# Kernel optimization log

Hardware: AMD Instinct MI355X
Metric: run time of the kernel (lower is better)

Reference implementation:

```python
import jax, jax.numpy as jnp
import numpy as np

N_USERS = 100000
N_ITEMS = 100000
EMB = 64
N_NODES = N_USERS + N_ITEMS + 2  # +1 padding row each for users and items
N_EDGES = 1200000
N_BEHAVIORS = 3
LAYERS = [3, 3, 3]
EPS = 1e-12  # F.normalize eps


def setup_inputs() -> dict:
    key = jax.random.key(0)
    k1, k2, k3, k4, k5 = jax.random.split(key, 5)
    user_emb = jax.random.normal(k1, (N_USERS + 1, EMB), dtype=jnp.float32)
    item_emb = jax.random.normal(k2, (N_ITEMS + 1, EMB), dtype=jnp.float32)
    rows = jax.random.randint(k3, (N_BEHAVIORS, N_EDGES), 0, N_NODES, dtype=jnp.int32)
    cols = jax.random.randint(k4, (N_BEHAVIORS, N_EDGES), 0, N_NODES, dtype=jnp.int32)
    weights = jax.random.uniform(k5, (N_BEHAVIORS, N_EDGES), dtype=jnp.float32)
    return {"user_emb": user_emb, "item_emb": item_emb, "rows": rows,
            "cols": cols, "weights": weights}


def _spmm(rows_b, cols_b, w_b, x):
    # sparse [N,N] @ dense [N,D] via gather + segment-sum (COO SpMM)
    msg = x[cols_b] * w_b[:, None]                      # [E, D]
    return jax.ops.segment_sum(msg, rows_b, num_segments=N_NODES)


def _l2_normalize(x):
    norm = jnp.sqrt(jnp.sum(x * x, axis=-1, keepdims=True))
    return x / jnp.maximum(norm, EPS)


def reference(user_emb, item_emb, rows, cols, weights):
    # NSED.gcn_propagate: sequential LightGCN per behavior with residual chaining
    total = jnp.concatenate([user_emb, item_emb], axis=0)  # [N, D]
    outs = []
    for b in range(N_BEHAVIORS):
        x = total
        acc = x            # running sum of layer embeddings (== mean of stack)
        for _ in range(LAYERS[b]):
            x = _spmm(rows[b], cols[b], weights[b], x)
            acc = acc + x
        lightgcn_emb = acc / jnp.float32(LAYERS[b] + 1)    # stack+mean over layers
        total = _l2_normalize(lightgcn_emb) + total
        outs.append(total)
    return jnp.stack(outs, axis=0)  # [B, N, D]
```

## Files before the change

### kernel.cpp

```cpp
#include <hip/hip_runtime.h>
#include <math.h>

#define N_USERS 100000
#define N_ITEMS 100000
#define EMB 64
#define N_NODES (N_USERS + N_ITEMS + 2)
#define N_EDGES 1200000
#define E3 (3 * N_EDGES)
#define N3 (3 * N_NODES)
#define ND ((long)N_NODES * (long)EMB)

#define KPB 1024
#define NBUCKET ((N3 + KPB - 1) / KPB)
#define CAP 6656
#define EPB 8192
#define SCT 512
#define NB_P1 ((E3 + EPB - 1) / EPB)

typedef float f32x4 __attribute__((ext_vector_type(4)));
typedef float f32x8 __attribute__((ext_vector_type(8)));
typedef unsigned short u16x4 __attribute__((ext_vector_type(4)));
typedef unsigned short u16x8 __attribute__((ext_vector_type(8)));

__device__ inline unsigned short f2bf(float f) {
    unsigned int u = __float_as_uint(f);
    return (unsigned short)((u + 0x7FFFu + ((u >> 16) & 1u)) >> 16);
}
__device__ inline void fma8(f32x8& acc, float w, u16x8 s) {
    #pragma unroll
    for (int j = 0; j < 8; ++j)
        acc[j] = fmaf(w, __uint_as_float((unsigned int)s[j] << 16), acc[j]);
}
__device__ inline f32x8 bf8_to_f8(u16x8 s) {
    f32x8 f;
    #pragma unroll
    for (int j = 0; j < 8; ++j) f[j] = __uint_as_float((unsigned int)s[j] << 16);
    return f;
}
__device__ inline u16x8 f8_to_bf8(f32x8 f) {
    u16x8 s;
    #pragma unroll
    for (int j = 0; j < 8; ++j) s[j] = f2bf(f[j]);
    return s;
}

__global__ void make_tb_kernel(const float4* __restrict__ u,
                               const float4* __restrict__ it,
                               u16x4* __restrict__ tb) {
    long i = (long)blockIdx.x * blockDim.x + threadIdx.x;
    if (i >= ND / 4) return;
    long n = i >> 4;
    float4 v = (n < (long)(N_USERS + 1)) ? u[i] : it[i - (long)(N_USERS + 1) * 16];
    u16x4 b;
    b.x = f2bf(v.x); b.y = f2bf(v.y); b.z = f2bf(v.z); b.w = f2bf(v.w);
    tb[i] = b;
}

__global__ void init_bcur_kernel(int* __restrict__ bcur, unsigned int* __restrict__ sedge) {
    int i = blockIdx.x * blockDim.x + threadIdx.x;
    if (i < NBUCKET) bcur[i] = i * CAP;
    if (i < 16) sedge[E3 + i] = 0u;
}

__global__ void bucket_scatter_kernel(const int* __restrict__ rows,
                                      const int* __restrict__ cols,
                                      const float* __restrict__ w,
                                      int* __restrict__ bcur,
                                      int2* __restrict__ tmpedge) {
    __shared__ int h[NBUCKET];
    __shared__ int lbase[NBUCKET];
    for (int i = threadIdx.x; i < NBUCKET; i += SCT) h[i] = 0;
    __syncthreads();
    long base = (long)blockIdx.x * EPB;
    int keys[EPB / SCT];
    for (int k = 0; k < EPB / SCT; ++k) {
        long e = base + k * SCT + threadIdx.x;
        int key = -1;
        if (e < E3) {
            int b = (e >= 2L * N_EDGES) ? 2 : ((e >= N_EDGES) ? 1 : 0);
            key = b * N_NODES + rows[e];
            atomicAdd(&h[key / KPB], 1);
        }
        keys[k] = key;
    }
    __syncthreads();
    for (int i = threadIdx.x; i < NBUCKET; i += SCT) {
        int c = h[i];
        lbase[i] = c ? atomicAdd(&bcur[i], c) : 0;
        h[i] = 0;
    }
    __syncthreads();
    for (int k = 0; k < EPB / SCT; ++k) {
        long e = base + k * SCT + threadIdx.x;
        int key = keys[k];
        if (key >= 0) {
            int bk = key / KPB;
            int pos = lbase[bk] + atomicAdd(&h[bk], 1);
            int2 pk;
            pk.x = ((key & (KPB - 1)) << 18) | cols[e];
            pk.y = __float_as_int(w[e]);
            tmpedge[pos] = pk;
        }
    }
}

__global__ void bucket_scan_kernel(const int* __restrict__ bcur, int* __restrict__ bbase,
                                   int* __restrict__ rowptr) {
    __shared__ int sm[1024];
    __shared__ int carry;
    int tid = threadIdx.x;
    if (tid == 0) carry = 0;
    __syncthreads();
    for (int base = 0; base < NBUCKET; base += 1024) {
        int i = base + tid;
        int v = (i < NBUCKET) ? (bcur[i] - i * CAP) : 0;
        sm[tid] = v;
        __syncthreads();
        for (int off = 1; off < 1024; off <<= 1) {
            int t = (tid >= off) ? sm[tid - off] : 0;
            __syncthreads();
            sm[tid] += t;
            __syncthreads();
        }
        if (i < NBUCKET) bbase[i] = sm[tid] - v + carry;
        __syncthreads();
        if (tid == 0) carry += sm[1023];
        __syncthreads();
    }
    if (tid == 0) { bbase[NBUCKET] = E3; rowptr[N3] = E3; }
}

__global__ void bucket_sort_kernel(const int* __restrict__ bbase,
                                   const int2* __restrict__ tmpedge,
                                   unsigned int* __restrict__ sedge,
                                   int* __restrict__ rowptr) {
    int g = blockIdx.x;
    int s = bbase[g];
    int cnt = bbase[g + 1] - s;
    long tb = (long)g * CAP;
    __shared__ int h[KPB];
    __shared__ int ex[KPB];
    __shared__ int tmp[512];
    int tid = threadIdx.x;
    h[tid * 2] = 0; h[tid * 2 + 1] = 0;
    __syncthreads();
    for (int i = tid; i < cnt; i += 512) atomicAdd(&h[tmpedge[tb + i].x >> 18], 1);
    __syncthreads();
    int a0 = h[tid * 2], a1 = h[tid * 2 + 1];
    int psum = a0 + a1;
    tmp[tid] = psum;
    __syncthreads();
    for (int off = 1; off < 512; off <<= 1) {
        int t = (tid >= off) ? tmp[tid - off] : 0;
        __syncthreads();
        tmp[tid] += t;
        __syncthreads();
    }
    int pex = tmp[tid] - psum;
    ex[tid * 2] = pex;
    ex[tid * 2 + 1] = pex + a0;
    __syncthreads();
    for (int j = tid; j < KPB; j += 512) {
        int key = g * KPB + j;
        if (key < N3) rowptr[key] = s + ex[j];
    }
    h[tid * 2] = ex[tid * 2];
    h[tid * 2 + 1] = ex[tid * 2 + 1];
    __syncthreads();
    for (int i = tid; i < cnt; i += 512) {
        int2 pk = tmpedge[tb + i];
        int kl = pk.x >> 18;
        int pos = s + atomicAdd(&h[kl], 1);
        float w = __int_as_float(pk.y);
        int wq = (int)fmaf(w, 16384.f, 0.5f);
        wq = wq > 16383 ? 16383 : (wq < 0 ? 0 : wq);
        sedge[pos] = ((unsigned int)(pk.x & 0x3FFFF) << 14) | (unsigned int)wq;
    }
}

__global__ void spmm_bf16_kernel(const int* __restrict__ rowptr,
                                 const unsigned int* __restrict__ sedge,
                                 const u16x8* __restrict__ x,
                                 u16x8* __restrict__ y) {
    int wid  = threadIdx.x >> 6;
    int lane = threadIdx.x & 63;
    int r = lane >> 3;
    int q = lane & 7;
    int n = (blockIdx.x * 4 + wid) * 8 + r;
    if (n >= N_NODES) return;
    int s = rowptr[n], e = rowptr[n + 1];
    f32x8 acc = {0.f, 0.f, 0.f, 0.f, 0.f, 0.f, 0.f, 0.f};
    for (int base = s; ; base += 8) {
        unsigned int ee[8];
        u16x8 bb[8];
        float ww[8];
        #pragma unroll
        for (int j = 0; j < 8; ++j) ee[j] = sedge[base + j];
        #pragma unroll
        for (int j = 0; j < 8; ++j) {
            bool valid = (base + j) < e;
            int c = valid ? (int)(ee[j] >> 14) : 0;
            ww[j] = valid ? (float)(ee[j] & 16383u) * (1.0f / 16384.0f) : 0.f;
            bb[j] = x[(long)c * 8 + q];
        }
        #pragma unroll
        for (int j = 0; j < 8; ++j) fma8(acc, ww[j], bb[j]);
        if (base + 8 >= e) break;
    }
    __builtin_nontemporal_store(f8_to_bf8(acc), &y[(long)n * 8 + q]);
}

__global__ void spmm_final_kernel(const int* __restrict__ rowptr,
                                  const unsigned int* __restrict__ sedge,
                                  const u16x8* __restrict__ Qb,
                                  const float* __restrict__ Tin,
                                  const float* __restrict__ uemb,
                                  const float* __restrict__ iemb,
                                  const u16x8* __restrict__ Pb,
                                  float* __restrict__ outp,
                                  u16x8* __restrict__ TbOut) {
    int wid  = threadIdx.x >> 6;
    int lane = threadIdx.x & 63;
    int r = lane >> 3;
    int q = lane & 7;
    int n = (blockIdx.x * 4 + wid) * 8 + r;
    if (n >= N_NODES) return;
    int s = rowptr[n], e = rowptr[n + 1];
    f32x8 acc = {0.f, 0.f, 0.f, 0.f, 0.f, 0.f, 0.f, 0.f};
    for (int base = s; ; base += 8) {
        unsigned int ee[8];
        u16x8 bb[8];
        float ww[8];
        #pragma unroll
        for (int j = 0; j < 8; ++j) ee[j] = sedge[base + j];
        #pragma unroll
        for (int j = 0; j < 8; ++j) {
            bool valid = (base + j) < e;
            int c = valid ? (int)(ee[j] >> 14) : 0;
            ww[j] = valid ? (float)(ee[j] & 16383u) * (1.0f / 16384.0f) : 0.f;
            bb[j] = Qb[(long)c * 8 + q];
        }
        #pragma unroll
        for (int j = 0; j < 8; ++j) fma8(acc, ww[j], bb[j]);
        if (base + 8 >= e) break;
    }
    const float* tsrc;
    if (Tin) tsrc = Tin + (long)n * EMB;
    else if (n <= N_USERS) tsrc = uemb + (long)n * EMB;
    else tsrc = iemb + (long)(n - N_USERS - 1) * EMB;
    long o = (long)n * 8 + q;
    f32x8 t = *(const f32x8*)(tsrc + q * 8);
    f32x8 p = bf8_to_f8(Pb[o]);
    f32x8 qv = bf8_to_f8(Qb[o]);
    f32x8 v;
    float ss = 0.f;
    #pragma unroll
    for (int j = 0; j < 8; ++j) {
        v[j] = (t[j] + p[j] + qv[j] + acc[j]) * 0.25f;
        ss = fmaf(v[j], v[j], ss);
    }
    ss += __shfl_xor(ss, 1, 64);
    ss += __shfl_xor(ss, 2, 64);
    ss += __shfl_xor(ss, 4, 64);
    float inv = 1.0f / fmaxf(sqrtf(ss), 1e-12f);
    f32x8 ov;
    #pragma unroll
    for (int j = 0; j < 8; ++j) ov[j] = fmaf(v[j], inv, t[j]);
    __builtin_nontemporal_store(ov, (f32x8*)(outp + (long)n * EMB + q * 8));
    if (TbOut) __builtin_nontemporal_store(f8_to_bf8(ov), &TbOut[o]);
}

extern "C" void kernel_launch(void* const* d_in, const int* in_sizes, int n_in,
                              void* d_out, int out_size, void* d_ws, size_t ws_size,
                              hipStream_t stream) {
    const float* user_emb = (const float*)d_in[0];
    const float* item_emb = (const float*)d_in[1];
    const int*   rows     = (const int*)d_in[2];
    const int*   cols     = (const int*)d_in[3];
    const float* weights  = (const float*)d_in[4];
    float* out = (float*)d_out;

    unsigned short* Tb   = (unsigned short*)d_ws;
    unsigned short* Pq   = Tb + ND;
    unsigned short* Qq   = Pq + ND;
    int2* tmpedge = (int2*)(Qq + ND);
    unsigned int* sedge = (unsigned int*)(tmpedge + (long)NBUCKET * CAP);
    int*  rowptr  = (int*)(sedge + E3 + 16);
    int*  bbase   = rowptr + N3 + 2;
    int*  bcur    = bbase + NBUCKET + 2;

    float* o0 = out;
    float* o1 = out + ND;
    float* o2 = out + 2 * ND;

    const long v4_blocks  = (ND / 4 + 255) / 256;
    const long row_blocks = ((long)N_NODES + 31) / 32;

    init_bcur_kernel<<<(NBUCKET + 255) / 256, 256, 0, stream>>>(bcur, sedge);
    bucket_scatter_kernel<<<NB_P1, SCT, 0, stream>>>(rows, cols, weights, bcur, tmpedge);
    bucket_scan_kernel<<<1, 1024, 0, stream>>>(bcur, bbase, rowptr);
    bucket_sort_kernel<<<NBUCKET, 512, 0, stream>>>(bbase, tmpedge, sedge, rowptr);

    make_tb_kernel<<<v4_blocks, 256, 0, stream>>>((const float4*)user_emb,
                                                  (const float4*)item_emb, (u16x4*)Tb);

    const float* Tins[3] = { nullptr, o0, o1 };
    float*       Dsts[3] = { o0, o1, o2 };

    for (int b = 0; b < 3; ++b) {
        const int* rp = rowptr + (long)b * N_NODES;
        u16x8* Pb = (u16x8*)Pq;
        u16x8* Qb = (u16x8*)Qq;

        spmm_bf16_kernel<<<row_blocks, 256, 0, stream>>>(rp, sedge, (const u16x8*)Tb, Pb);
        spmm_bf16_kernel<<<row_blocks, 256, 0, stream>>>(rp, sedge, (const u16x8*)Pb, Qb);
        spmm_final_kernel<<<row_blocks, 256, 0, stream>>>(rp, sedge, (const u16x8*)Qb,
                                                          Tins[b], user_emb, item_emb,
                                                          (const u16x8*)Pb, Dsts[b],
                                                          (b < 2) ? (u16x8*)Tb : nullptr);
    }
}
```

Baseline: 415.7 us.

## Bin rows by degree class and process SpMM rows through a degree-sorted permutation

Adds a histogram, offset and scatter pass that groups each behavior's rows into four degree classes (by number of 8-edge chunks) and writes a permutation array. The SpMM kernels then map each 8-lane group to a row taken from this permutation, so rows sharing a wavefront have similar edge counts. The aim is to cut divergence and idle lanes from the variable-length loop. The cost is three extra small kernels plus atomics, an extra indirection load per row, and scattered output writes and rowptr reads that lose their sequential locality.

After: 460.8 us. 10.9% more time.

```diff
diff --git a/kernel.cpp b/kernel.cpp
--- a/kernel.cpp
+++ b/kernel.cpp
@@ -16,6 +16,7 @@
 #define EPB 8192
 #define SCT 512
 #define NB_P1 ((E3 + EPB - 1) / EPB)
+#define NCLS 12
 
 typedef float f32x4 __attribute__((ext_vector_type(4)));
 typedef float f32x8 __attribute__((ext_vector_type(8)));
@@ -56,10 +57,12 @@
     tb[i] = b;
 }
 
-__global__ void init_bcur_kernel(int* __restrict__ bcur, unsigned int* __restrict__ sedge) {
+__global__ void init_bcur_kernel(int* __restrict__ bcur, unsigned int* __restrict__ sedge,
+                                 int* __restrict__ ccnt) {
     int i = blockIdx.x * blockDim.x + threadIdx.x;
     if (i < NBUCKET) bcur[i] = i * CAP;
     if (i < 16) sedge[E3 + i] = 0u;
+    if (i < NCLS) ccnt[i] = 0;
 }
 
 __global__ void bucket_scatter_kernel(const int* __restrict__ rows,
@@ -178,7 +181,64 @@
     }
 }
 
+__device__ inline int deg_class(int i, const int* rowptr) {
+    int d = rowptr[i + 1] - rowptr[i];
+    int c = (d + 7) >> 3;
+    return c > 3 ? 3 : c;
+}
+
+__global__ void deg_hist_kernel(const int* __restrict__ rowptr, int* __restrict__ ccnt) {
+    __shared__ int h[NCLS];
+    if (threadIdx.x < NCLS) h[threadIdx.x] = 0;
+    __syncthreads();
+    int i = blockIdx.x * blockDim.x + threadIdx.x;
+    if (i < N3) {
+        int cls = (i / N_NODES) * 4 + deg_class(i, rowptr);
+        atomicAdd(&h[cls], 1);
+    }
+    __syncthreads();
+    if (threadIdx.x < NCLS) {
+        int v = h[threadIdx.x];
+        if (v) atomicAdd(&ccnt[threadIdx.x], v);
+    }
+}
+
+__global__ void deg_offset_kernel(const int* __restrict__ ccnt, int* __restrict__ gcur) {
+    if (threadIdx.x == 0) {
+        for (int b = 0; b < 3; ++b) {
+            int off = b * N_NODES;
+            for (int c = 0; c < 4; ++c) { gcur[b * 4 + c] = off; off += ccnt[b * 4 + c]; }
+        }
+    }
+}
+
+__global__ void deg_scatter_kernel(const int* __restrict__ rowptr, int* __restrict__ gcur,
+                                   int* __restrict__ perm) {
+    __shared__ int h[NCLS], lbase[NCLS];
+    int tid = threadIdx.x;
+    if (tid < NCLS) h[tid] = 0;
+    __syncthreads();
+    int i = blockIdx.x * blockDim.x + tid;
+    int cls = -1;
+    if (i < N3) {
+        cls = (i / N_NODES) * 4 + deg_class(i, rowptr);
+        atomicAdd(&h[cls], 1);
+    }
+    __syncthreads();
+    if (tid < NCLS) {
+        int v = h[tid];
+        lbase[tid] = v ? atomicAdd(&gcur[tid], v) : 0;
+        h[tid] = 0;
+    }
+    __syncthreads();
+    if (cls >= 0) {
+        int pos = lbase[cls] + atomicAdd(&h[cls], 1);
+        perm[pos] = i - (cls >> 2) * N_NODES;
+    }
+}
+
 __global__ void spmm_bf16_kernel(const int* __restrict__ rowptr,
+                                 const int* __restrict__ perm,
                                  const unsigned int* __restrict__ sedge,
                                  const u16x8* __restrict__ x,
                                  u16x8* __restrict__ y) {
@@ -186,8 +246,9 @@
     int lane = threadIdx.x & 63;
     int r = lane >> 3;
     int q = lane & 7;
-    int n = (blockIdx.x * 4 + wid) * 8 + r;
-    if (n >= N_NODES) return;
+    int slot = (blockIdx.x * 4 + wid) * 8 + r;
+    if (slot >= N_NODES) return;
+    int n = perm[slot];
     int s = rowptr[n], e = rowptr[n + 1];
     f32x8 acc = {0.f, 0.f, 0.f, 0.f, 0.f, 0.f, 0.f, 0.f};
     for (int base = s; ; base += 8) {
@@ -211,6 +272,7 @@
 }
 
 __global__ void spmm_final_kernel(const int* __restrict__ rowptr,
+                                  const int* __restrict__ perm,
                                   const unsigned int* __restrict__ sedge,
                                   const u16x8* __restrict__ Qb,
                                   const float* __restrict__ Tin,
@@ -223,8 +285,9 @@
     int lane = threadIdx.x & 63;
     int r = lane >> 3;
     int q = lane & 7;
-    int n = (blockIdx.x * 4 + wid) * 8 + r;
-    if (n >= N_NODES) return;
+    int slot = (blockIdx.x * 4 + wid) * 8 + r;
+    if (slot >= N_NODES) return;
+    int n = perm[slot];
     int s = rowptr[n], e = rowptr[n + 1];
     f32x8 acc = {0.f, 0.f, 0.f, 0.f, 0.f, 0.f, 0.f, 0.f};
     for (int base = s; ; base += 8) {
@@ -288,6 +351,9 @@
     int*  rowptr  = (int*)(sedge + E3 + 16);
     int*  bbase   = rowptr + N3 + 2;
     int*  bcur    = bbase + NBUCKET + 2;
+    int*  ccnt    = bcur + NBUCKET;
+    int*  gcur    = ccnt + NCLS;
+    int*  perm    = gcur + NCLS;
 
     float* o0 = out;
     float* o1 = out + ND;
@@ -295,12 +361,17 @@
 
     const long v4_blocks  = (ND / 4 + 255) / 256;
     const long row_blocks = ((long)N_NODES + 31) / 32;
-
-    init_bcur_kernel<<<(NBUCKET + 255) / 256, 256, 0, stream>>>(bcur, sedge);
+    const long n3_blocks  = (N3 + 511) / 512;
+
+    init_bcur_kernel<<<(NBUCKET + 255) / 256, 256, 0, stream>>>(bcur, sedge, ccnt);
     bucket_scatter_kernel<<<NB_P1, SCT, 0, stream>>>(rows, cols, weights, bcur, tmpedge);
     bucket_scan_kernel<<<1, 1024, 0, stream>>>(bcur, bbase, rowptr);
     bucket_sort_kernel<<<NBUCKET, 512, 0, stream>>>(bbase, tmpedge, sedge, rowptr);
 
+    deg_hist_kernel<<<n3_blocks, 512, 0, stream>>>(rowptr, ccnt);
+    deg_offset_kernel<<<1, 64, 0, stream>>>(ccnt, gcur);
+    deg_scatter_kernel<<<n3_blocks, 512, 0, stream>>>(rowptr, gcur, perm);
+
     make_tb_kernel<<<v4_blocks, 256, 0, stream>>>((const float4*)user_emb,
                                                   (const float4*)item_emb, (u16x4*)Tb);
 
@@ -309,12 +380,15 @@
 
     for (int b = 0; b < 3; ++b) {
         const int* rp = rowptr + (long)b * N_NODES;
+        const int* pm = perm + (long)b * N_NODES;
         u16x8* Pb = (u16x8*)Pq;
         u16x8* Qb = (u16x8*)Qq;
 
-        spmm_bf16_kernel<<<row_blocks, 256, 0, stream>>>(rp, sedge, (const u16x8*)Tb, Pb);
-        spmm_bf16_kernel<<<row_blocks, 256, 0, stream>>>(rp, sedge, (const u16x8*)Pb, Qb);
-        spmm_final_kernel<<<row_blocks, 256, 0, stream>>>(rp, sedge, (const u16x8*)Qb,
+        spmm_bf16_kernel<<<row_blocks, 256, 0, stream>>>(rp, pm, sedge,
+                                                         (const u16x8*)Tb, Pb);
+        spmm_bf16_kernel<<<row_blocks, 256, 0, stream>>>(rp, pm, sedge,
+                                                         (const u16x8*)Pb, Qb);
+        spmm_final_kernel<<<row_blocks, 256, 0, stream>>>(rp, pm, sedge, (const u16x8*)Qb,
                                                           Tins[b], user_emb, item_emb,
                                                           (const u16x8*)Pb, Dsts[b],
                                                           (b < 2) ? (u16x8*)Tb : nullptr);
```
